# Performance work log

Measured on AMD Instinct MI355X. Metric: run time of the kernel, lower is better.

Reference implementation:

```python
import jax, jax.numpy as jnp
import numpy as np

CHUNK = 256
THETA = 10000.0

def rope2d(x):
    # x: (b, h, n, d), d divisible by 4
    b, h, n, d = x.shape
    pad = (-n) % CHUNK
    if pad:
        x = jnp.pad(x, ((0, 0), (0, 0), (0, pad), (0, 0)))
    c = (n + pad) // CHUNK
    x = x.reshape(b, h, c, CHUNK, d)
    inv = 1.0 / THETA ** (jnp.arange(0, d, 4, dtype=jnp.float32) / d)  # (d/4,)
    fl = jnp.arange(CHUNK, dtype=jnp.float32)[:, None] * inv[None, :]  # (l, d/4)
    cos_l, sin_l = jnp.cos(fl), jnp.sin(fl)
    fc = jnp.arange(c, dtype=jnp.float32)[:, None] * inv[None, :]      # (c, d/4)
    cos_c, sin_c = jnp.cos(fc)[:, None, :], jnp.sin(fc)[:, None, :]    # (c, 1, d/4)
    x1, x2, x3, x4 = jnp.split(x, 4, axis=-1)
    r1 = x1 * cos_l - x2 * sin_l
    r2 = x1 * sin_l + x2 * cos_l
    r3 = x3 * cos_c - x4 * sin_c
    r4 = x3 * sin_c + x4 * cos_c
    out = jnp.concatenate([r1, r2, r3, r4], axis=-1).reshape(b, h, c * CHUNK, d)
    return out[:, :, :n]


def setup_inputs():
    key = jax.random.key(0)
    ks = jax.random.split(key, 6)
    dim, heads = 512, 8
    b, n = 2, 2048
    s = 0.02
    return {
        'x': jax.random.normal(ks[0], (b, n, dim), dtype=jnp.float32),
        'w_qkv': jax.random.normal(ks[1], (3 * dim, dim), dtype=jnp.float32) * s,
        'b_qkv': jnp.zeros((3 * dim,), dtype=jnp.float32),
        'w_pre': jax.random.normal(ks[2], (heads, heads), dtype=jnp.float32) * 0.3,
        'w_post': jax.random.normal(ks[3], (heads, heads), dtype=jnp.float32) * 0.3,
        'w_out': jax.random.normal(ks[4], (dim, dim), dtype=jnp.float32) * s,
        'b_out': jnp.zeros((dim,), dtype=jnp.float32),
    }


def reference(x, w_qkv, b_qkv, w_pre, w_post, w_out, b_out):
    b, n, dim = x.shape
    heads = w_pre.shape[0]
    d = dim // heads
    scale = d ** -0.5
    qkv = x @ w_qkv.T + b_qkv                      # (b, n, 3*dim)
    q, k, v = jnp.split(qkv, 3, axis=-1)
    def to_heads(t):
        return t.reshape(b, n, heads, d).transpose(0, 2, 1, 3)  # (b, h, n, d)
    q, k, v = to_heads(q), to_heads(k), to_heads(v)
    q = rope2d(q)
    k = rope2d(k)
    logits = jnp.einsum('bhid,bhjd->bhij', q, k) * scale
    # talking-heads pre-softmax mix (Linear over head dim, no bias)
    logits = jnp.einsum('bhij,gh->bgij', logits, w_pre)
    attn = jax.nn.softmax(logits, axis=-1)
    # post-softmax mix
    attn = jnp.einsum('bhij,gh->bgij', attn, w_post)
    out = jnp.einsum('bhij,bhjd->bhid', attn, v)   # (b, h, n, d)
    out = out.transpose(0, 2, 1, 3).reshape(b, n, dim)
    return out @ w_out.T + b_out
```

## Files before the change

### kernel.cpp

```cpp
#include <hip/hip_runtime.h>
#include <hip/hip_bf16.h>

typedef __attribute__((ext_vector_type(8))) short bf16x8;
typedef __attribute__((ext_vector_type(4))) float f32x4;

#define DEV static __device__ __forceinline__

DEV unsigned short f2bf(float f) {
    __hip_bfloat16 h = __float2bfloat16(f);
    return __builtin_bit_cast(unsigned short, h);
}
DEV float bf2f(unsigned short s) {
    union { unsigned int u; float f; } v; v.u = ((unsigned int)s) << 16; return v.f;
}
DEV bf16x8 ld_bf8(const unsigned short* p) { return *reinterpret_cast<const bf16x8*>(p); }
DEV f32x4 mfma16(bf16x8 a, bf16x8 b, f32x4 c) {
    return __builtin_amdgcn_mfma_f32_16x16x32_bf16(a, b, c, 0, 0, 0);
}

__global__ __launch_bounds__(256) void k_qkv(
    const float* __restrict__ xf, const float* __restrict__ wf,
    const float* __restrict__ bias,
    unsigned short* __restrict__ Qb, unsigned short* __restrict__ Kb,
    unsigned short* __restrict__ Vt)
{
    __shared__ unsigned short As[64][40];
    __shared__ unsigned short Bs[64][40];
    const int m0 = blockIdx.x * 64, c0 = blockIdx.y * 64;
    const int t = threadIdx.x;
    const int w = t >> 6, lane = t & 63, li = lane & 15, lg = lane >> 4;
    const int wr = w >> 1, wc = w & 1;
    f32x4 acc[2][2] = {};
    const int srow = t >> 2, spart = (t & 3) * 8;
    for (int kt = 0; kt < 512; kt += 32) {
        const float* xs = &xf[(size_t)(m0 + srow) * 512 + kt + spart];
        float4 a0 = *(const float4*)xs, a1 = *(const float4*)(xs + 4);
        const float* wsrc = &wf[(size_t)(c0 + srow) * 512 + kt + spart];
        float4 b0 = *(const float4*)wsrc, b1 = *(const float4*)(wsrc + 4);
        ushort4 ua0 = { f2bf(a0.x), f2bf(a0.y), f2bf(a0.z), f2bf(a0.w) };
        ushort4 ua1 = { f2bf(a1.x), f2bf(a1.y), f2bf(a1.z), f2bf(a1.w) };
        ushort4 ub0 = { f2bf(b0.x), f2bf(b0.y), f2bf(b0.z), f2bf(b0.w) };
        ushort4 ub1 = { f2bf(b1.x), f2bf(b1.y), f2bf(b1.z), f2bf(b1.w) };
        *(ushort4*)&As[srow][spart] = ua0; *(ushort4*)&As[srow][spart + 4] = ua1;
        *(ushort4*)&Bs[srow][spart] = ub0; *(ushort4*)&Bs[srow][spart + 4] = ub1;
        __syncthreads();
        bf16x8 af[2], bfr[2];
        #pragma unroll
        for (int mf = 0; mf < 2; mf++) af[mf] = ld_bf8(&As[wr*32 + mf*16 + li][lg*8]);
        #pragma unroll
        for (int nf = 0; nf < 2; nf++) bfr[nf] = ld_bf8(&Bs[wc*32 + nf*16 + li][lg*8]);
        #pragma unroll
        for (int mf = 0; mf < 2; mf++)
            #pragma unroll
            for (int nf = 0; nf < 2; nf++)
                acc[mf][nf] = mfma16(af[mf], bfr[nf], acc[mf][nf]);
        __syncthreads();
    }
    const int type = c0 >> 9;
    const int head = (c0 & 511) >> 6;
    const float b0s = bias[c0 + wc*32 + li];
    const float b1s = bias[c0 + wc*32 + 16 + li];
    float invf = 0.f;
    if (type < 2) invf = powf(10000.f, -(float)li * (1.f/16.f));
    #pragma unroll
    for (int mf = 0; mf < 2; mf++) {
        #pragma unroll
        for (int r = 0; r < 4; r++) {
            int grow = m0 + wr*32 + mf*16 + lg*4 + r;
            int tok = grow & 2047, bb = grow >> 11;
            float v0 = acc[mf][0][r] + b0s;
            float v1 = acc[mf][1][r] + b1s;
            if (type < 2) {
                float ang = (wc == 0 ? (float)(tok & 255) : (float)(tok >> 8)) * invf;
                float s, c;
                sincosf(ang, &s, &c);
                float r0 = v0 * c - v1 * s;
                float r1 = v0 * s + v1 * c;
                unsigned short* dst = (type == 0 ? Qb : Kb);
                size_t base = (((size_t)(bb*8 + head)) * 2048 + tok) * 64 + wc*32 + li;
                dst[base]      = f2bf(r0);
                dst[base + 16] = f2bf(r1);
            } else {
                size_t base = (((size_t)(bb*8 + head)) * 64 + wc*32 + li) * 2048 + tok;
                Vt[base]             = f2bf(v0);
                Vt[base + 16 * 2048] = f2bf(v1);
            }
        }
    }
}

#define SCALE_L2E (0.125f * 1.44269504088896340736f)

#define STAGE_Q() do { \
    for (int v = threadIdx.x; v < 1024; v += 512) { \
        int h_ = v >> 7, rest_ = v & 127, i_ = rest_ >> 3, ch_ = rest_ & 7; \
        *(uint4*)&Qlds[h_][i_][ch_*8] = \
            *(const uint4*)&Qb[(((size_t)(bb*8 + h_))*2048 + i0 + i_)*64 + ch_*8]; \
    } \
} while (0)

#define QK_ALLH() do { \
    _Pragma("unroll") for (int h = 0; h < 8; h++) { \
        const unsigned short* kp_ = Kb + (((size_t)(bb*8 + h))*2048 + js + li)*64; \
        bf16x8 k0_ = ld_bf8(kp_ + lg*8), k1_ = ld_bf8(kp_ + 32 + lg*8); \
        bf16x8 q0_ = ld_bf8(&Qlds[h][li][lg*8]); \
        bf16x8 q1_ = ld_bf8(&Qlds[h][li][32 + lg*8]); \
        f32x4 z_ = {}; \
        z_ = mfma16(q0_, k0_, z_); \
        acc[h] = mfma16(q1_, k1_, z_); \
    } \
} while (0)

__global__ __launch_bounds__(512, 4) void k_lsum(
    const unsigned short* __restrict__ Qb, const unsigned short* __restrict__ Kb,
    const float* __restrict__ w_pre, float* __restrict__ Lp)
{
    __shared__ unsigned short Qlds[8][16][72];
    __shared__ float Red[8][128];
    const int orig = blockIdx.x;
    const int virt = ((orig & 7) << 6) | (orig >> 3);
    const int jh = virt & 1, it = (virt >> 1) & 127, bb = virt >> 8;
    const int i0 = it * 16;
    const int tid = threadIdx.x, w = tid >> 6, lane = tid & 63, li = lane & 15, lg = lane >> 4;
    STAGE_Q();
    __syncthreads();
    float lacc[4][8] = {};
    #pragma unroll 1
    for (int s = 0; s < 8; s++) {
        const int js = jh*1024 + s*128 + w*16;
        f32x4 acc[8];
        QK_ALLH();
        #pragma unroll
        for (int r = 0; r < 4; r++) {
            #pragma unroll
            for (int a = 0; a < 8; a++) {
                float t = 0.f;
                #pragma unroll
                for (int h = 0; h < 8; h++) t = fmaf(w_pre[a*8 + h], acc[h][r], t);
                lacc[r][a] += __builtin_amdgcn_exp2f(t * SCALE_L2E);
            }
        }
    }
    #pragma unroll
    for (int m = 1; m <= 8; m <<= 1)
        #pragma unroll
        for (int r = 0; r < 4; r++)
            #pragma unroll
            for (int a = 0; a < 8; a++)
                lacc[r][a] += __shfl_xor(lacc[r][a], m);
    if (li == 0) {
        #pragma unroll
        for (int r = 0; r < 4; r++)
            #pragma unroll
            for (int a = 0; a < 8; a++)
                Red[w][(lg*4 + r)*8 + a] = lacc[r][a];
    }
    __syncthreads();
    if (tid < 128) {
        float s = 0.f;
        #pragma unroll
        for (int ww = 0; ww < 8; ww++) s += Red[ww][tid];
        float* Lpw = Lp + (size_t)jh * 32768;
        Lpw[((size_t)bb*2048 + i0 + (tid >> 3))*8 + (tid & 7)] = s;
    }
}

__global__ __launch_bounds__(512, 4) void k_attn(
    const unsigned short* __restrict__ Qb, const unsigned short* __restrict__ Kb,
    const unsigned short* __restrict__ Vt,
    const float* __restrict__ w_pre, const float* __restrict__ w_post,
    const float* __restrict__ Lp,
    unsigned short* __restrict__ AOp0, unsigned short* __restrict__ AOp1)
{
    __shared__ unsigned short Qlds[8][16][72];
    __shared__ unsigned short Ah[8][16][136];
    __shared__ float Llds[128];
    const int orig = blockIdx.x;
    const int virt = ((orig & 7) << 6) | (orig >> 3);
    const int jh = virt & 1, it = (virt >> 1) & 127, bb = virt >> 8;
    const int i0 = it * 16;
    const int tid = threadIdx.x, w = tid >> 6, lane = tid & 63, li = lane & 15, lg = lane >> 4;
    STAGE_Q();
    if (tid < 128) {
        int i_ = tid >> 3, a_ = tid & 7;
        size_t g = ((size_t)bb*2048 + i0 + i_)*8 + a_;
        Llds[a_*16 + i_] = __builtin_amdgcn_logf(Lp[g] + Lp[32768 + g]);
    }
    const unsigned short* Vp = Vt + ((size_t)(bb*8 + w)) * 64 * 2048;
    __syncthreads();
    f32x4 oacc[4] = {};
    #pragma unroll 1
    for (int s = 0; s < 8; s++) {
        const int j0 = jh*1024 + s*128;
        const int js = j0 + w*16;
        f32x4 acc[8];
        QK_ALLH();
        if (s > 0) {
            const int jp = j0 - 128;
            #pragma unroll
            for (int kc = 0; kc < 4; kc++) {
                bf16x8 pa = ld_bf8(&Ah[w][li][kc*32 + lg*8]);
                #pragma unroll
                for (int nf = 0; nf < 4; nf++) {
                    bf16x8 vfr = ld_bf8(Vp + (size_t)(nf*16 + li)*2048 + jp + kc*32 + lg*8);
                    oacc[nf] = mfma16(pa, vfr, oacc[nf]);
                }
            }
        }
        unsigned short a2s[4][8];
        #pragma unroll
        for (int r = 0; r < 4; r++) {
            float p[8];
            #pragma unroll
            for (int a = 0; a < 8; a++) {
                float t = 0.f;
                #pragma unroll
                for (int h = 0; h < 8; h++) t = fmaf(w_pre[a*8 + h], acc[h][r], t);
                p[a] = __builtin_amdgcn_exp2f(t * SCALE_L2E - Llds[a*16 + lg*4 + r]);
            }
            #pragma unroll
            for (int c = 0; c < 8; c++) {
                float t = 0.f;
                #pragma unroll
                for (int a = 0; a < 8; a++) t = fmaf(w_post[c*8 + a], p[a], t);
                a2s[r][c] = f2bf(t);
            }
        }
        __syncthreads();
        #pragma unroll
        for (int r = 0; r < 4; r++)
            #pragma unroll
            for (int c = 0; c < 8; c++)
                Ah[c][lg*4 + r][w*16 + li] = a2s[r][c];
        __syncthreads();
    }
    {
        const int jp = jh*1024 + 7*128;
        #pragma unroll
        for (int kc = 0; kc < 4; kc++) {
            bf16x8 pa = ld_bf8(&Ah[w][li][kc*32 + lg*8]);
            #pragma unroll
            for (int nf = 0; nf < 4; nf++) {
                bf16x8 vfr = ld_bf8(Vp + (size_t)(nf*16 + li)*2048 + jp + kc*32 + lg*8);
                oacc[nf] = mfma16(pa, vfr, oacc[nf]);
            }
        }
    }
    unsigned short* ao = jh ? AOp1 : AOp0;
    #pragma unroll
    for (int nf = 0; nf < 4; nf++)
        #pragma unroll
        for (int r = 0; r < 4; r++)
            ao[((size_t)bb*2048 + i0 + lg*4 + r)*512 + w*64 + nf*16 + li] = f2bf(oacc[nf][r]);
}

__global__ __launch_bounds__(256) void k_out(
    const unsigned short* __restrict__ a0, const unsigned short* __restrict__ a1,
    const float* __restrict__ wf, const float* __restrict__ bias,
    float* __restrict__ out)
{
    __shared__ unsigned short As[64][40];
    __shared__ unsigned short Bs[64][40];
    const int m0 = blockIdx.x * 64, c0 = blockIdx.y * 64;
    const int t = threadIdx.x;
    const int w = t >> 6, lane = t & 63, li = lane & 15, lg = lane >> 4;
    const int wr = w >> 1, wc = w & 1;
    f32x4 acc[2][2] = {};
    const int srow = t >> 2, spart = (t & 3) * 8;
    for (int kt = 0; kt < 512; kt += 32) {
        size_t aidx = (size_t)(m0 + srow) * 512 + kt + spart;
        uint4 ua = *(const uint4*)&a0[aidx];
        uint4 ub = *(const uint4*)&a1[aidx];
        const unsigned short* pa = (const unsigned short*)&ua;
        const unsigned short* pb = (const unsigned short*)&ub;
        unsigned short us[8];
        #pragma unroll
        for (int q = 0; q < 8; q++) us[q] = f2bf(bf2f(pa[q]) + bf2f(pb[q]));
        *reinterpret_cast<uint4*>(&As[srow][spart]) = *(const uint4*)us;
        const float* wsrc = &wf[(size_t)(c0 + srow) * 512 + kt + spart];
        float4 b0 = *(const float4*)wsrc, b1 = *(const float4*)(wsrc + 4);
        ushort4 ub0 = { f2bf(b0.x), f2bf(b0.y), f2bf(b0.z), f2bf(b0.w) };
        ushort4 ub1 = { f2bf(b1.x), f2bf(b1.y), f2bf(b1.z), f2bf(b1.w) };
        *(ushort4*)&Bs[srow][spart] = ub0; *(ushort4*)&Bs[srow][spart + 4] = ub1;
        __syncthreads();
        bf16x8 af[2], bfr[2];
        #pragma unroll
        for (int mf = 0; mf < 2; mf++) af[mf] = ld_bf8(&As[wr*32 + mf*16 + li][lg*8]);
        #pragma unroll
        for (int nf = 0; nf < 2; nf++) bfr[nf] = ld_bf8(&Bs[wc*32 + nf*16 + li][lg*8]);
        #pragma unroll
        for (int mf = 0; mf < 2; mf++)
            #pragma unroll
            for (int nf = 0; nf < 2; nf++)
                acc[mf][nf] = mfma16(af[mf], bfr[nf], acc[mf][nf]);
        __syncthreads();
    }
    #pragma unroll
    for (int mf = 0; mf < 2; mf++)
        #pragma unroll
        for (int nf = 0; nf < 2; nf++)
            #pragma unroll
            for (int r = 0; r < 4; r++) {
                int grow = m0 + wr*32 + mf*16 + lg*4 + r;
                int gcol = c0 + wc*32 + nf*16 + li;
                out[(size_t)grow * 512 + gcol] = acc[mf][nf][r] + bias[gcol];
            }
}

extern "C" void kernel_launch(void* const* d_in, const int* in_sizes, int n_in,
                              void* d_out, int out_size, void* d_ws, size_t ws_size,
                              hipStream_t stream)
{
    const float* x      = (const float*)d_in[0];
    const float* w_qkv  = (const float*)d_in[1];
    const float* b_qkv  = (const float*)d_in[2];
    const float* w_pre  = (const float*)d_in[3];
    const float* w_post = (const float*)d_in[4];
    const float* w_out  = (const float*)d_in[5];
    const float* b_out  = (const float*)d_in[6];
    float* out = (float*)d_out;

    char* ws = (char*)d_ws;
    unsigned short* Qb   = (unsigned short*)(ws);
    unsigned short* Kb   = (unsigned short*)(ws + 4194304);
    unsigned short* Vt   = (unsigned short*)(ws + 8388608);
    unsigned short* AOp0 = (unsigned short*)(ws + 12582912);
    unsigned short* AOp1 = (unsigned short*)(ws + 16777216);
    float* Lp            = (float*)(ws + 20971520);

    k_qkv<<<dim3(64, 24), 256, 0, stream>>>(x, w_qkv, b_qkv, Qb, Kb, Vt);
    k_lsum<<<512, 512, 0, stream>>>(Qb, Kb, w_pre, Lp);
    k_attn<<<512, 512, 0, stream>>>(Qb, Kb, Vt, w_pre, w_post, Lp, AOp0, AOp1);
    k_out<<<dim3(64, 8), 256, 0, stream>>>(AOp0, AOp1, w_out, b_out, out);
}
```

Baseline: 247.3 us.

## Swap QK MFMA operands, keep P in registers via bpermute, split lsum into quarters

The QK MFMA now computes S transposed, so each lane holds one query row. That lets the softmax log-sum live in per-lane registers and the P matrix be passed to the PV MFMA through ds_bpermute rather than an LDS round trip with two barriers per step. Each wave now handles a 32-key slab for all 8 output heads and keeps 8x4 accumulators. A cross-wave LDS reduction runs at the end, and the k_lsum grid is doubled to four key quarters to add parallelism. The cost is much higher register pressure (occupancy hint lowered to 2) and a final reduction with 16 barriers.

```diff
diff --git a/kernel.cpp b/kernel.cpp
--- a/kernel.cpp
+++ b/kernel.cpp
@@ -17,6 +17,8 @@
 DEV f32x4 mfma16(bf16x8 a, bf16x8 b, f32x4 c) {
     return __builtin_amdgcn_mfma_f32_16x16x32_bf16(a, b, c, 0, 0, 0);
 }
+
+#define SCALE_L2E (0.125f * 1.44269504088896340736f)
 
 __global__ __launch_bounds__(256) void k_qkv(
     const float* __restrict__ xf, const float* __restrict__ wf,
@@ -89,8 +91,6 @@
     }
 }
 
-#define SCALE_L2E (0.125f * 1.44269504088896340736f)
-
 #define STAGE_Q() do { \
     for (int v = threadIdx.x; v < 1024; v += 512) { \
         int h_ = v >> 7, rest_ = v & 127, i_ = rest_ >> 3, ch_ = rest_ & 7; \
@@ -99,73 +99,71 @@
     } \
 } while (0)
 
-#define QK_ALLH() do { \
+#define QK_SWAPPED(JT) do { \
     _Pragma("unroll") for (int h = 0; h < 8; h++) { \
-        const unsigned short* kp_ = Kb + (((size_t)(bb*8 + h))*2048 + js + li)*64; \
+        const unsigned short* kp_ = Kbase + ((size_t)h*2048 + js + (JT)*16 + li)*64; \
         bf16x8 k0_ = ld_bf8(kp_ + lg*8), k1_ = ld_bf8(kp_ + 32 + lg*8); \
         bf16x8 q0_ = ld_bf8(&Qlds[h][li][lg*8]); \
         bf16x8 q1_ = ld_bf8(&Qlds[h][li][32 + lg*8]); \
         f32x4 z_ = {}; \
-        z_ = mfma16(q0_, k0_, z_); \
-        acc[h] = mfma16(q1_, k1_, z_); \
+        z_ = mfma16(k0_, q0_, z_); \
+        sT[h] = mfma16(k1_, q1_, z_); \
     } \
 } while (0)
 
-__global__ __launch_bounds__(512, 4) void k_lsum(
+__global__ __launch_bounds__(512) void k_lsum(
     const unsigned short* __restrict__ Qb, const unsigned short* __restrict__ Kb,
     const float* __restrict__ w_pre, float* __restrict__ Lp)
 {
     __shared__ unsigned short Qlds[8][16][72];
-    __shared__ float Red[8][128];
+    __shared__ float Red2[8][16][9];
     const int orig = blockIdx.x;
-    const int virt = ((orig & 7) << 6) | (orig >> 3);
-    const int jh = virt & 1, it = (virt >> 1) & 127, bb = virt >> 8;
+    const int virt = ((orig & 7) << 7) | (orig >> 3);
+    const int it = virt & 127, jq = (virt >> 7) & 3, bb = virt >> 9;
     const int i0 = it * 16;
     const int tid = threadIdx.x, w = tid >> 6, lane = tid & 63, li = lane & 15, lg = lane >> 4;
     STAGE_Q();
     __syncthreads();
-    float lacc[4][8] = {};
+    const unsigned short* Kbase = Kb + (size_t)bb * 8 * 2048 * 64;
+    float lacc[8] = {};
     #pragma unroll 1
-    for (int s = 0; s < 8; s++) {
-        const int js = jh*1024 + s*128 + w*16;
-        f32x4 acc[8];
-        QK_ALLH();
-        #pragma unroll
-        for (int r = 0; r < 4; r++) {
-            #pragma unroll
-            for (int a = 0; a < 8; a++) {
-                float t = 0.f;
-                #pragma unroll
-                for (int h = 0; h < 8; h++) t = fmaf(w_pre[a*8 + h], acc[h][r], t);
-                lacc[r][a] += __builtin_amdgcn_exp2f(t * SCALE_L2E);
-            }
+    for (int s = 0; s < 2; s++) {
+        const int js = jq*512 + s*256 + w*32;
+        #pragma unroll
+        for (int jt = 0; jt < 2; jt++) {
+            f32x4 sT[8];
+            QK_SWAPPED(jt);
+            #pragma unroll
+            for (int r = 0; r < 4; r++)
+                #pragma unroll
+                for (int a = 0; a < 8; a++) {
+                    float t = 0.f;
+                    #pragma unroll
+                    for (int h = 0; h < 8; h++) t = fmaf(w_pre[a*8 + h], sT[h][r], t);
+                    lacc[a] += __builtin_amdgcn_exp2f(t * SCALE_L2E);
+                }
         }
     }
     #pragma unroll
-    for (int m = 1; m <= 8; m <<= 1)
-        #pragma unroll
-        for (int r = 0; r < 4; r++)
-            #pragma unroll
-            for (int a = 0; a < 8; a++)
-                lacc[r][a] += __shfl_xor(lacc[r][a], m);
-    if (li == 0) {
-        #pragma unroll
-        for (int r = 0; r < 4; r++)
-            #pragma unroll
-            for (int a = 0; a < 8; a++)
-                Red[w][(lg*4 + r)*8 + a] = lacc[r][a];
+    for (int a = 0; a < 8; a++) {
+        lacc[a] += __shfl_xor(lacc[a], 16);
+        lacc[a] += __shfl_xor(lacc[a], 32);
+    }
+    if (lg == 0) {
+        #pragma unroll
+        for (int a = 0; a < 8; a++) Red2[w][li][a] = lacc[a];
     }
     __syncthreads();
     if (tid < 128) {
-        float s = 0.f;
-        #pragma unroll
-        for (int ww = 0; ww < 8; ww++) s += Red[ww][tid];
-        float* Lpw = Lp + (size_t)jh * 32768;
-        Lpw[((size_t)bb*2048 + i0 + (tid >> 3))*8 + (tid & 7)] = s;
-    }
-}
-
-__global__ __launch_bounds__(512, 4) void k_attn(
+        const int i_ = tid >> 3, a_ = tid & 7;
+        float sv = 0.f;
+        #pragma unroll
+        for (int ww = 0; ww < 8; ww++) sv += Red2[ww][i_][a_];
+        Lp[(size_t)jq*32768 + ((size_t)bb*2048 + i0 + i_)*8 + a_] = sv;
+    }
+}
+
+__global__ __launch_bounds__(512, 2) void k_attn(
     const unsigned short* __restrict__ Qb, const unsigned short* __restrict__ Kb,
     const unsigned short* __restrict__ Vt,
     const float* __restrict__ w_pre, const float* __restrict__ w_post,
@@ -173,85 +171,116 @@
     unsigned short* __restrict__ AOp0, unsigned short* __restrict__ AOp1)
 {
     __shared__ unsigned short Qlds[8][16][72];
-    __shared__ unsigned short Ah[8][16][136];
-    __shared__ float Llds[128];
+    __shared__ float Red[8][16][68];
     const int orig = blockIdx.x;
     const int virt = ((orig & 7) << 6) | (orig >> 3);
-    const int jh = virt & 1, it = (virt >> 1) & 127, bb = virt >> 8;
+    const int it = virt & 127, jh = (virt >> 7) & 1, bb = virt >> 8;
     const int i0 = it * 16;
     const int tid = threadIdx.x, w = tid >> 6, lane = tid & 63, li = lane & 15, lg = lane >> 4;
     STAGE_Q();
-    if (tid < 128) {
-        int i_ = tid >> 3, a_ = tid & 7;
-        size_t g = ((size_t)bb*2048 + i0 + i_)*8 + a_;
-        Llds[a_*16 + i_] = __builtin_amdgcn_logf(Lp[g] + Lp[32768 + g]);
-    }
-    const unsigned short* Vp = Vt + ((size_t)(bb*8 + w)) * 64 * 2048;
+    float Llog[8];
+    {
+        const size_t gL = ((size_t)bb*2048 + i0 + li) * 8;
+        #pragma unroll
+        for (int a = 0; a < 8; a++)
+            Llog[a] = __builtin_amdgcn_logf(
+                Lp[gL + a] + Lp[32768 + gL + a] + Lp[65536 + gL + a] + Lp[98304 + gL + a]);
+    }
+    const unsigned short* Kbase = Kb + (size_t)bb * 8 * 2048 * 64;
+    const unsigned short* Vbase = Vt + (size_t)bb * 8 * 64 * 2048;
     __syncthreads();
-    f32x4 oacc[4] = {};
+    const int idx0 = (((lane >> 4) & 1) * 32 + li) * 4;
+    const int idx1 = idx0 + 64;
+    const bool jthi = (lane & 32) != 0;
+    f32x4 oacc[8][4] = {};
     #pragma unroll 1
-    for (int s = 0; s < 8; s++) {
-        const int j0 = jh*1024 + s*128;
-        const int js = j0 + w*16;
-        f32x4 acc[8];
-        QK_ALLH();
-        if (s > 0) {
-            const int jp = j0 - 128;
-            #pragma unroll
-            for (int kc = 0; kc < 4; kc++) {
-                bf16x8 pa = ld_bf8(&Ah[w][li][kc*32 + lg*8]);
-                #pragma unroll
-                for (int nf = 0; nf < 4; nf++) {
-                    bf16x8 vfr = ld_bf8(Vp + (size_t)(nf*16 + li)*2048 + jp + kc*32 + lg*8);
-                    oacc[nf] = mfma16(pa, vfr, oacc[nf]);
+    for (int s = 0; s < 4; s++) {
+        const int js = jh*1024 + s*256 + w*32;
+        unsigned pkw[8][4];
+        #pragma unroll
+        for (int jt = 0; jt < 2; jt++) {
+            f32x4 sT[8];
+            QK_SWAPPED(jt);
+            #pragma unroll
+            for (int r = 0; r < 4; r++) {
+                float p[8];
+                #pragma unroll
+                for (int a = 0; a < 8; a++) {
+                    float t = 0.f;
+                    #pragma unroll
+                    for (int h = 0; h < 8; h++) t = fmaf(w_pre[a*8 + h], sT[h][r], t);
+                    p[a] = __builtin_amdgcn_exp2f(t * SCALE_L2E - Llog[a]);
                 }
-            }
-        }
-        unsigned short a2s[4][8];
-        #pragma unroll
-        for (int r = 0; r < 4; r++) {
-            float p[8];
-            #pragma unroll
-            for (int a = 0; a < 8; a++) {
-                float t = 0.f;
-                #pragma unroll
-                for (int h = 0; h < 8; h++) t = fmaf(w_pre[a*8 + h], acc[h][r], t);
-                p[a] = __builtin_amdgcn_exp2f(t * SCALE_L2E - Llds[a*16 + lg*4 + r]);
-            }
-            #pragma unroll
-            for (int c = 0; c < 8; c++) {
-                float t = 0.f;
-                #pragma unroll
-                for (int a = 0; a < 8; a++) t = fmaf(w_post[c*8 + a], p[a], t);
-                a2s[r][c] = f2bf(t);
-            }
-        }
-        __syncthreads();
-        #pragma unroll
-        for (int r = 0; r < 4; r++)
-            #pragma unroll
-            for (int c = 0; c < 8; c++)
-                Ah[c][lg*4 + r][w*16 + li] = a2s[r][c];
-        __syncthreads();
-    }
-    {
-        const int jp = jh*1024 + 7*128;
-        #pragma unroll
-        for (int kc = 0; kc < 4; kc++) {
-            bf16x8 pa = ld_bf8(&Ah[w][li][kc*32 + lg*8]);
-            #pragma unroll
-            for (int nf = 0; nf < 4; nf++) {
-                bf16x8 vfr = ld_bf8(Vp + (size_t)(nf*16 + li)*2048 + jp + kc*32 + lg*8);
-                oacc[nf] = mfma16(pa, vfr, oacc[nf]);
+                #pragma unroll
+                for (int c = 0; c < 8; c++) {
+                    float t = 0.f;
+                    #pragma unroll
+                    for (int a = 0; a < 8; a++) t = fmaf(w_post[c*8 + a], p[a], t);
+                    const unsigned bv = f2bf(t);
+                    if (r & 1) pkw[c][jt*2 + (r >> 1)] |= (bv << 16);
+                    else       pkw[c][jt*2 + (r >> 1)]  = bv;
+                }
+            }
+        }
+        bf16x8 vc[4];
+        #pragma unroll
+        for (int nf = 0; nf < 4; nf++)
+            vc[nf] = ld_bf8(Vbase + ((size_t)(nf*16 + li))*2048 + js + lg*8);
+        #pragma unroll
+        for (int c = 0; c < 8; c++) {
+            bf16x8 vn[4];
+            if (c < 7) {
+                #pragma unroll
+                for (int nf = 0; nf < 4; nf++)
+                    vn[nf] = ld_bf8(Vbase + ((size_t)((c+1)*64 + nf*16 + li))*2048 + js + lg*8);
+            }
+            union { unsigned u[4]; bf16x8 v; } af;
+            {
+                const int p0 = __builtin_amdgcn_ds_bpermute(idx0, (int)pkw[c][0]);
+                const int p2 = __builtin_amdgcn_ds_bpermute(idx0, (int)pkw[c][2]);
+                const int p1 = __builtin_amdgcn_ds_bpermute(idx0, (int)pkw[c][1]);
+                const int p3 = __builtin_amdgcn_ds_bpermute(idx0, (int)pkw[c][3]);
+                const int q0 = __builtin_amdgcn_ds_bpermute(idx1, (int)pkw[c][0]);
+                const int q2 = __builtin_amdgcn_ds_bpermute(idx1, (int)pkw[c][2]);
+                const int q1 = __builtin_amdgcn_ds_bpermute(idx1, (int)pkw[c][1]);
+                const int q3 = __builtin_amdgcn_ds_bpermute(idx1, (int)pkw[c][3]);
+                af.u[0] = (unsigned)(jthi ? p2 : p0);
+                af.u[1] = (unsigned)(jthi ? p3 : p1);
+                af.u[2] = (unsigned)(jthi ? q2 : q0);
+                af.u[3] = (unsigned)(jthi ? q3 : q1);
+            }
+            #pragma unroll
+            for (int nf = 0; nf < 4; nf++)
+                oacc[c][nf] = mfma16(af.v, vc[nf], oacc[c][nf]);
+            if (c < 7) {
+                #pragma unroll
+                for (int nf = 0; nf < 4; nf++) vc[nf] = vn[nf];
             }
         }
     }
     unsigned short* ao = jh ? AOp1 : AOp0;
-    #pragma unroll
-    for (int nf = 0; nf < 4; nf++)
-        #pragma unroll
-        for (int r = 0; r < 4; r++)
-            ao[((size_t)bb*2048 + i0 + lg*4 + r)*512 + w*64 + nf*16 + li] = f2bf(oacc[nf][r]);
+    #pragma unroll 1
+    for (int c = 0; c < 8; c++) {
+        __syncthreads();
+        #pragma unroll
+        for (int nf = 0; nf < 4; nf++)
+            #pragma unroll
+            for (int r = 0; r < 4; r++)
+                Red[w][lg*4 + r][nf*16 + li] = oacc[c][nf][r];
+        __syncthreads();
+        {
+            const int i_ = tid >> 6, d_ = tid & 63;
+            float sv = 0.f;
+            #pragma unroll
+            for (int ww = 0; ww < 8; ww++) sv += Red[ww][i_][d_];
+            ao[((size_t)bb*2048 + i0 + i_)*512 + c*64 + d_] = f2bf(sv);
+            const int i2 = (tid + 512) >> 6;
+            float sv2 = 0.f;
+            #pragma unroll
+            for (int ww = 0; ww < 8; ww++) sv2 += Red[ww][i2][d_];
+            ao[((size_t)bb*2048 + i0 + i2)*512 + c*64 + d_] = f2bf(sv2);
+        }
+    }
 }
 
 __global__ __launch_bounds__(256) void k_out(
@@ -329,7 +358,7 @@
     float* Lp            = (float*)(ws + 20971520);
 
     k_qkv<<<dim3(64, 24), 256, 0, stream>>>(x, w_qkv, b_qkv, Qb, Kb, Vt);
-    k_lsum<<<512, 512, 0, stream>>>(Qb, Kb, w_pre, Lp);
+    k_lsum<<<1024, 512, 0, stream>>>(Qb, Kb, w_pre, Lp);
     k_attn<<<512, 512, 0, stream>>>(Qb, Kb, Vt, w_pre, w_post, Lp, AOp0, AOp1);
     k_out<<<dim3(64, 8), 256, 0, stream>>>(AOp0, AOp1, w_out, b_out, out);
 }
```

Result: slower. 360.6 us (+45.8%).

## Halve attention-probability LDS buffer and pair softmax mixing into float2 ops

Applied to the files above, without the earlier changes.

The talking-heads pre/post mix loops now process two rows at once with float2 accumulators, which may let the compiler emit packed FMA instructions. In k_attn the Ah shared buffer is halved to 4 heads, and each step is split into two LDS write/sync/PV phases run by waves 0-3 and then 4-7. The one-step software pipelining of PV behind the next QK is removed. This cuts LDS use to allow more resident blocks, at the cost of extra barriers, half the waves idling during each PV phase, and less overlap.

```diff
diff --git a/kernel.cpp b/kernel.cpp
--- a/kernel.cpp
+++ b/kernel.cpp
@@ -3,6 +3,7 @@
 
 typedef __attribute__((ext_vector_type(8))) short bf16x8;
 typedef __attribute__((ext_vector_type(4))) float f32x4;
+typedef __attribute__((ext_vector_type(2))) float f32x2;
 
 #define DEV static __device__ __forceinline__
 
@@ -17,6 +18,8 @@
 DEV f32x4 mfma16(bf16x8 a, bf16x8 b, f32x4 c) {
     return __builtin_amdgcn_mfma_f32_16x16x32_bf16(a, b, c, 0, 0, 0);
 }
+
+#define SCALE_L2E (0.125f * 1.44269504088896340736f)
 
 __global__ __launch_bounds__(256) void k_qkv(
     const float* __restrict__ xf, const float* __restrict__ wf,
@@ -89,8 +92,6 @@
     }
 }
 
-#define SCALE_L2E (0.125f * 1.44269504088896340736f)
-
 #define STAGE_Q() do { \
     for (int v = threadIdx.x; v < 1024; v += 512) { \
         int h_ = v >> 7, rest_ = v & 127, i_ = rest_ >> 3, ch_ = rest_ & 7; \
@@ -131,13 +132,18 @@
         f32x4 acc[8];
         QK_ALLH();
         #pragma unroll
-        for (int r = 0; r < 4; r++) {
+        for (int r2 = 0; r2 < 2; r2++) {
             #pragma unroll
             for (int a = 0; a < 8; a++) {
-                float t = 0.f;
-                #pragma unroll
-                for (int h = 0; h < 8; h++) t = fmaf(w_pre[a*8 + h], acc[h][r], t);
-                lacc[r][a] += __builtin_amdgcn_exp2f(t * SCALE_L2E);
+                f32x2 t = {0.f, 0.f};
+                #pragma unroll
+                for (int h = 0; h < 8; h++) {
+                    const float wv = w_pre[a*8 + h];
+                    t.x = fmaf(wv, acc[h][2*r2], t.x);
+                    t.y = fmaf(wv, acc[h][2*r2 + 1], t.y);
+                }
+                lacc[2*r2][a]     += __builtin_amdgcn_exp2f(t.x * SCALE_L2E);
+                lacc[2*r2 + 1][a] += __builtin_amdgcn_exp2f(t.y * SCALE_L2E);
             }
         }
     }
@@ -173,7 +179,7 @@
     unsigned short* __restrict__ AOp0, unsigned short* __restrict__ AOp1)
 {
     __shared__ unsigned short Qlds[8][16][72];
-    __shared__ unsigned short Ah[8][16][136];
+    __shared__ unsigned short Ah[4][16][136];
     __shared__ float Llds[128];
     const int orig = blockIdx.x;
     const int virt = ((orig & 7) << 6) | (orig >> 3);
@@ -195,54 +201,70 @@
         const int js = j0 + w*16;
         f32x4 acc[8];
         QK_ALLH();
-        if (s > 0) {
-            const int jp = j0 - 128;
+        unsigned short a2s[4][8];
+        #pragma unroll
+        for (int r2 = 0; r2 < 2; r2++) {
+            f32x2 p2[8];
+            #pragma unroll
+            for (int a = 0; a < 8; a++) {
+                f32x2 t = {0.f, 0.f};
+                #pragma unroll
+                for (int h = 0; h < 8; h++) {
+                    const float wv = w_pre[a*8 + h];
+                    t.x = fmaf(wv, acc[h][2*r2], t.x);
+                    t.y = fmaf(wv, acc[h][2*r2 + 1], t.y);
+                }
+                const f32x2 lgv = *(const f32x2*)&Llds[a*16 + lg*4 + 2*r2];
+                p2[a].x = __builtin_amdgcn_exp2f(t.x * SCALE_L2E - lgv.x);
+                p2[a].y = __builtin_amdgcn_exp2f(t.y * SCALE_L2E - lgv.y);
+            }
+            #pragma unroll
+            for (int c = 0; c < 8; c++) {
+                f32x2 t = {0.f, 0.f};
+                #pragma unroll
+                for (int a = 0; a < 8; a++) {
+                    const float wv = w_post[c*8 + a];
+                    t.x = fmaf(wv, p2[a].x, t.x);
+                    t.y = fmaf(wv, p2[a].y, t.y);
+                }
+                a2s[2*r2][c]     = f2bf(t.x);
+                a2s[2*r2 + 1][c] = f2bf(t.y);
+            }
+        }
+        __syncthreads();
+        #pragma unroll
+        for (int r = 0; r < 4; r++)
+            #pragma unroll
+            for (int c = 0; c < 4; c++)
+                Ah[c][lg*4 + r][w*16 + li] = a2s[r][c];
+        __syncthreads();
+        if (w < 4) {
             #pragma unroll
             for (int kc = 0; kc < 4; kc++) {
                 bf16x8 pa = ld_bf8(&Ah[w][li][kc*32 + lg*8]);
                 #pragma unroll
                 for (int nf = 0; nf < 4; nf++) {
-                    bf16x8 vfr = ld_bf8(Vp + (size_t)(nf*16 + li)*2048 + jp + kc*32 + lg*8);
+                    bf16x8 vfr = ld_bf8(Vp + (size_t)(nf*16 + li)*2048 + j0 + kc*32 + lg*8);
                     oacc[nf] = mfma16(pa, vfr, oacc[nf]);
                 }
             }
         }
-        unsigned short a2s[4][8];
-        #pragma unroll
-        for (int r = 0; r < 4; r++) {
-            float p[8];
-            #pragma unroll
-            for (int a = 0; a < 8; a++) {
-                float t = 0.f;
-                #pragma unroll
-                for (int h = 0; h < 8; h++) t = fmaf(w_pre[a*8 + h], acc[h][r], t);
-                p[a] = __builtin_amdgcn_exp2f(t * SCALE_L2E - Llds[a*16 + lg*4 + r]);
-            }
-            #pragma unroll
-            for (int c = 0; c < 8; c++) {
-                float t = 0.f;
-                #pragma unroll
-                for (int a = 0; a < 8; a++) t = fmaf(w_post[c*8 + a], p[a], t);
-                a2s[r][c] = f2bf(t);
-            }
-        }
-        __syncthreads();
-        #pragma unroll
-        for (int r = 0; r < 4; r++)
-            #pragma unroll
-            for (int c = 0; c < 8; c++)
-                Ah[c][lg*4 + r][w*16 + li] = a2s[r][c];
-        __syncthreads();
-    }
-    {
-        const int jp = jh*1024 + 7*128;
-        #pragma unroll
-        for (int kc = 0; kc < 4; kc++) {
-            bf16x8 pa = ld_bf8(&Ah[w][li][kc*32 + lg*8]);
-            #pragma unroll
-            for (int nf = 0; nf < 4; nf++) {
-                bf16x8 vfr = ld_bf8(Vp + (size_t)(nf*16 + li)*2048 + jp + kc*32 + lg*8);
-                oacc[nf] = mfma16(pa, vfr, oacc[nf]);
+        __syncthreads();
+        #pragma unroll
+        for (int r = 0; r < 4; r++)
+            #pragma unroll
+            for (int c = 0; c < 4; c++)
+                Ah[c][lg*4 + r][w*16 + li] = a2s[r][c + 4];
+        __syncthreads();
+        if (w >= 4) {
+            #pragma unroll
+            for (int kc = 0; kc < 4; kc++) {
+                bf16x8 pa = ld_bf8(&Ah[w - 4][li][kc*32 + lg*8]);
+                #pragma unroll
+                for (int nf = 0; nf < 4; nf++) {
+                    bf16x8 vfr = ld_bf8(Vp + (size_t)(nf*16 + li)*2048 + j0 + kc*32 + lg*8);
+                    oacc[nf] = mfma16(pa, vfr, oacc[nf]);
+                }
             }
         }
     }
```

After: 247.7 us. Within noise of the previous version (+0.2%).
